# Performance work log

Hardware: AMD Instinct MI355X
Metric: run time of the kernel (lower is better)

Reference implementation:

```python
import jax, jax.numpy as jnp
import numpy as np

B, T, D, L, K = 16, 512, 256, 2, 3
MAX_OUT = 4096  # static padded output length = T * max_duration
LN_EPS = 1e-5


def setup_inputs() -> dict:
    key = jax.random.key(0)
    ks = jax.random.split(key, 8)
    x = jax.random.normal(ks[0], (B, T, D), dtype=jnp.float32)
    mfAlign = jax.random.randint(ks[1], (B, T), 0, 8, dtype=jnp.int32)  # integer frame durations
    pitch = jax.random.uniform(ks[2], (B, T), dtype=jnp.float32)
    energy = jax.random.uniform(ks[3], (B, T), dtype=jnp.float32)
    # duration Predictor params (2 conv layers + layernorms + final linear->1)
    conv_w = jax.random.normal(ks[4], (L, D, D, K), dtype=jnp.float32) * 0.02  # [layer, out, in, k]
    conv_b = jnp.zeros((L, D), dtype=jnp.float32)
    ln_g = jnp.ones((L, D), dtype=jnp.float32)
    ln_b = jnp.zeros((L, D), dtype=jnp.float32)
    lin_w = jax.random.normal(ks[5], (1, D), dtype=jnp.float32) * 0.02
    lin_b = jnp.zeros((1,), dtype=jnp.float32)
    return dict(x=x, mfAlign=mfAlign, pitch=pitch, energy=energy,
                conv_w=conv_w, conv_b=conv_b, ln_g=ln_g, ln_b=ln_b,
                lin_w=lin_w, lin_b=lin_b, max_out=MAX_OUT)


def _conv1d(h, w, b):
    # h: [B, T, D] -> NCW conv with same padding -> [B, T, D]
    y = jax.lax.conv_general_dilated(h.transpose(0, 2, 1), w, (1,), [(K // 2, K // 2)],
                                     dimension_numbers=('NCW', 'OIW', 'NCW'))
    return (y + b[None, :, None]).transpose(0, 2, 1)


def _layernorm(h, g, b):
    m = jnp.mean(h, axis=-1, keepdims=True)
    v = jnp.var(h, axis=-1, keepdims=True)
    return (h - m) * jax.lax.rsqrt(v + LN_EPS) * g + b


def _duration_predictor(h, conv_w, conv_b, ln_g, ln_b, lin_w, lin_b):
    # eval-mode Predictor: conv -> relu -> layernorm (dropout is identity at eval)
    for i in range(conv_w.shape[0]):
        h = _layernorm(jax.nn.relu(_conv1d(h, conv_w[i], conv_b[i])), ln_g[i], ln_b[i])
    return (h @ lin_w.T + lin_b)[..., 0]  # [B, T]


def _length_regulator(x, dur, max_out):
    # expand token t of batch b dur[b,t] times; pad each row to max_out
    dur = jnp.maximum(dur, 0)
    cum = jnp.cumsum(dur, axis=1)                 # [B, T]
    lengths = cum[:, -1]                          # [B]
    pos = jnp.arange(max_out, dtype=cum.dtype)    # [max_out]
    # output frame p of batch b copies token idx[b,p] = first t with cum[b,t] > p
    idx = jax.vmap(lambda c: jnp.searchsorted(c, pos, side='right'))(cum)
    idx = jnp.minimum(idx, x.shape[1] - 1)
    hidden = jnp.take_along_axis(x, idx[:, :, None], axis=1)   # [B, max_out, D]
    mask = (pos[None, :] < lengths[:, None])[:, :, None]
    return jnp.where(mask, hidden, jnp.zeros((), x.dtype)), lengths


def reference(x, mfAlign, pitch, energy, conv_w, conv_b, ln_g, ln_b, lin_w, lin_b, max_out):
    # VarianceAdaptor.forward with bGenerating=False
    lab = mfAlign.astype(x.dtype)
    d = _duration_predictor(jax.lax.stop_gradient(x), conv_w, conv_b, ln_g, ln_b, lin_w, lin_b)
    dLoss = jnp.mean((d - lab) ** 2)
    hiddenSeq, hiddenSeqLength = _length_regulator(x, mfAlign, max_out)
    return hiddenSeq, hiddenSeqLength, dLoss
```

## Files before the change

kernel.cpp:

```cpp
#include <hip/hip_runtime.h>
#include <hip/hip_bf16.h>

#define DD 256
#define TTT 512
#define BB 16
#define KK 3
#define MAXO 4096
#define LN_EPS 1e-5f
#define TPAD 514
#define NKT 24

typedef __attribute__((ext_vector_type(8))) short short8;
typedef __attribute__((ext_vector_type(4))) float f32x4;

static __device__ inline short bf16r(float v) {
    __hip_bfloat16 h = __float2bfloat16(v);
    return reinterpret_cast<short&>(h);
}

__global__ void k_prep_w(const float* __restrict__ w, short* __restrict__ wpk) {
    int tid = blockIdx.x * blockDim.x + threadIdx.x;
    if (tid >= 2 * NKT * 16 * 64) return;
    int lane = tid & 63;
    int rest = tid >> 6;
    int nf = rest & 15; rest >>= 4;
    int kt = rest % NKT;
    int l  = rest / NKT;
    int n     = nf * 16 + (lane & 15);
    int kbase = kt * 32 + (lane >> 4) * 8;
    short8 v;
#pragma unroll
    for (int j = 0; j < 8; ++j) {
        int k   = kbase + j;
        int kap = k >> 8;
        int i   = k & 255;
        v[j] = bf16r(w[(((l * DD) + n) * DD + i) * KK + kap]);
    }
    *reinterpret_cast<short8*>(wpk + (size_t)tid * 8) = v;
}

__global__ void k_prep_x(const float* __restrict__ x, short* __restrict__ xb,
                         short* __restrict__ h1b) {
    int tid = blockIdx.x * blockDim.x + threadIdx.x;
    if (tid >= BB * TPAD * DD) return;
    int r = (tid >> 8) % TPAD;
    if (r == 0 || r == TPAD - 1) {
        xb[tid] = 0; h1b[tid] = 0;
    } else {
        int c = tid & 255;
        int b = tid / (TPAD * DD);
        xb[tid] = bf16r(x[((size_t)b * TTT + (r - 1)) * DD + c]);
    }
}

__global__ void k_cumsum(const int* __restrict__ mf, int* __restrict__ cum,
                         float* __restrict__ dout, int* __restrict__ idxb) {
    __shared__ int s[TTT];
    int b = blockIdx.x, t = threadIdx.x;
    s[t] = mf[b * TTT + t];
    __syncthreads();
    for (int off = 1; off < TTT; off <<= 1) {
        int v = (t >= off) ? s[t - off] : 0;
        __syncthreads();
        s[t] += v;
        __syncthreads();
    }
    cum[b * TTT + t] = s[t];
    int hi = s[t];
    int lo = (t == 0) ? 0 : s[t - 1];
    for (int p = lo; p < hi; ++p) idxb[b * MAXO + p] = t;
    if (t == TTT - 1) dout[(size_t)BB * MAXO * DD + b] = (float)s[t];
    if (b == 0 && t == 0) dout[(size_t)BB * MAXO * DD + BB] = 0.f;
}

template <bool DO_LOSS>
__global__ __launch_bounds__(256) void k_conv_mfma(
    const short* __restrict__ ain,
    short* __restrict__ aout,
    const short8* __restrict__ bp,
    const float* __restrict__ cb,
    const float* __restrict__ g, const float* __restrict__ bvec,
    const float* __restrict__ lw, const float* __restrict__ lb,
    const int* __restrict__ mf, float* __restrict__ loss) {
    __shared__ float yt[16][260];
    int bt = blockIdx.x;
    int b  = bt >> 5;
    int t0 = (bt & 31) << 4;
    int tid = threadIdx.x;
    int lane = tid & 63, wv = tid >> 6;
    int mrow = lane & 15;
    int kg   = lane >> 4;

    const short* Ab = ain + ((size_t)b * TPAD + t0 + mrow) * DD + kg * 8;
    f32x4 acc0 = {0.f,0.f,0.f,0.f}, acc1 = acc0, acc2 = acc0, acc3 = acc0;
    const short8* bw = bp + (size_t)wv * 4 * 64 + lane;

    for (int kt = 0; kt < NKT; ++kt) {
        short8 a  = *reinterpret_cast<const short8*>(Ab + kt * 32);
        short8 b0 = bw[0];
        short8 b1 = bw[64];
        short8 b2 = bw[128];
        short8 b3 = bw[192];
        acc0 = __builtin_amdgcn_mfma_f32_16x16x32_bf16(a, b0, acc0, 0, 0, 0);
        acc1 = __builtin_amdgcn_mfma_f32_16x16x32_bf16(a, b1, acc1, 0, 0, 0);
        acc2 = __builtin_amdgcn_mfma_f32_16x16x32_bf16(a, b2, acc2, 0, 0, 0);
        acc3 = __builtin_amdgcn_mfma_f32_16x16x32_bf16(a, b3, acc3, 0, 0, 0);
        bw += 16 * 64;
    }

#define EPI(F, ACC) { int c = ((wv * 4 + F) << 4) + mrow; float bias = cb[c];   \
        yt[kg * 4 + 0][c] = fmaxf(ACC[0] + bias, 0.f);                          \
        yt[kg * 4 + 1][c] = fmaxf(ACC[1] + bias, 0.f);                          \
        yt[kg * 4 + 2][c] = fmaxf(ACC[2] + bias, 0.f);                          \
        yt[kg * 4 + 3][c] = fmaxf(ACC[3] + bias, 0.f); }
    EPI(0, acc0) EPI(1, acc1) EPI(2, acc2) EPI(3, acc3)
#undef EPI
    __syncthreads();

    float lsum = 0.f;
    int c0 = lane << 1;
#pragma unroll
    for (int q = 0; q < 4; ++q) {
        int r = wv * 4 + q;
        float2 vA = *reinterpret_cast<float2*>(&yt[r][c0]);
        float2 vB = *reinterpret_cast<float2*>(&yt[r][c0 + 128]);
        float s  = vA.x + vA.y + vB.x + vB.y;
        float s2 = vA.x*vA.x + vA.y*vA.y + vB.x*vB.x + vB.y*vB.y;
#pragma unroll
        for (int off = 1; off < 64; off <<= 1) {
            s  += __shfl_xor(s, off);
            s2 += __shfl_xor(s2, off);
        }
        float mean = s * (1.f / DD);
        float var  = s2 * (1.f / DD) - mean * mean;
        float rs   = rsqrtf(var + LN_EPS);
        float2 gA = *reinterpret_cast<const float2*>(&g[c0]);
        float2 gB = *reinterpret_cast<const float2*>(&g[c0 + 128]);
        float2 bA = *reinterpret_cast<const float2*>(&bvec[c0]);
        float2 bB = *reinterpret_cast<const float2*>(&bvec[c0 + 128]);
        float oAx = (vA.x - mean) * rs * gA.x + bA.x;
        float oAy = (vA.y - mean) * rs * gA.y + bA.y;
        float oBx = (vB.x - mean) * rs * gB.x + bB.x;
        float oBy = (vB.y - mean) * rs * gB.y + bB.y;
        if constexpr (!DO_LOSS) {
            size_t rowb = ((size_t)b * TPAD + t0 + r + 1) * DD;
            short2 sA, sB;
            sA.x = bf16r(oAx); sA.y = bf16r(oAy);
            sB.x = bf16r(oBx); sB.y = bf16r(oBy);
            *reinterpret_cast<short2*>(&aout[rowb + c0])       = sA;
            *reinterpret_cast<short2*>(&aout[rowb + c0 + 128]) = sB;
        } else {
            float2 lA = *reinterpret_cast<const float2*>(&lw[c0]);
            float2 lB = *reinterpret_cast<const float2*>(&lw[c0 + 128]);
            float p = oAx * lA.x + oAy * lA.y + oBx * lB.x + oBy * lB.y;
#pragma unroll
            for (int off = 1; off < 64; off <<= 1) p += __shfl_xor(p, off);
            if (lane == 0) {
                float dv = p + lb[0];
                float er = dv - (float)mf[b * TTT + t0 + r];
                lsum += er * er;
            }
        }
    }
    if constexpr (DO_LOSS) {
        if (lane == 0) atomicAdd(loss, lsum * (1.f / (BB * TTT)));
    }
}

__global__ __launch_bounds__(256) void k_lenreg2(const float* __restrict__ x,
                                                 const int* __restrict__ cum,
                                                 const int* __restrict__ idxb,
                                                 float* __restrict__ out) {
    int blk = blockIdx.x;
    int b   = blk >> 7;
    int p0  = (blk & 127) << 5;
    int tid = threadIdx.x;
    int lane = tid & 63, wv = tid >> 6;
    int len = cum[b * TTT + TTT - 1];
    const float4* x4 = (const float4*)x;
    float4* o4 = (float4*)out;
#pragma unroll
    for (int r = 0; r < 8; ++r) {
        int p = p0 + (wv << 3) + r;
        size_t oidx = ((size_t)b * MAXO + p) * 64 + lane;
        if (p < len) {
            int idx = idxb[b * MAXO + p];
            o4[oidx] = x4[((size_t)b * TTT + idx) * 64 + lane];
        } else {
            o4[oidx] = make_float4(0.f, 0.f, 0.f, 0.f);
        }
    }
}

extern "C" void kernel_launch(void* const* d_in, const int* in_sizes, int n_in,
                              void* d_out, int out_size, void* d_ws, size_t ws_size,
                              hipStream_t stream) {
    const float* x      = (const float*)d_in[0];
    const int*   mf     = (const int*)d_in[1];
    const float* conv_w = (const float*)d_in[4];
    const float* conv_b = (const float*)d_in[5];
    const float* ln_g   = (const float*)d_in[6];
    const float* ln_b   = (const float*)d_in[7];
    const float* lin_w  = (const float*)d_in[8];
    const float* lin_b  = (const float*)d_in[9];
    float* out = (float*)d_out;

    short* wpk = (short*)d_ws;
    short* xb  = wpk + (size_t)2 * NKT * 16 * 64 * 8;
    short* h1b = xb + (size_t)BB * TPAD * DD;
    int*   cum  = (int*)(h1b + (size_t)BB * TPAD * DD);
    int*   idxb = cum + BB * TTT;

    float* lossp = out + (size_t)BB * MAXO * DD + BB;

    k_prep_w<<<(2 * NKT * 16 * 64 + 255) / 256, 256, 0, stream>>>(conv_w, wpk);
    k_prep_x<<<(BB * TPAD * DD + 255) / 256, 256, 0, stream>>>(x, xb, h1b);
    k_cumsum<<<BB, TTT, 0, stream>>>(mf, cum, out, idxb);
    k_conv_mfma<false><<<BB * (TTT / 16), 256, 0, stream>>>(
        xb, h1b, (const short8*)wpk, conv_b, ln_g, ln_b,
        nullptr, nullptr, nullptr, nullptr);
    k_conv_mfma<true><<<BB * (TTT / 16), 256, 0, stream>>>(
        h1b, nullptr, (const short8*)wpk + (size_t)NKT * 16 * 64,
        conv_b + DD, ln_g + DD, ln_b + DD, lin_w, lin_b, mf, lossp);
    k_lenreg2<<<BB * (MAXO / 32), 256, 0, stream>>>(x, cum, idxb, out);
}
```

Measured before the change: 165.8 us.

## Merge prep kernels and co-schedule length regulator with first conv layer

```diff
diff --git a/kernel.cpp b/kernel.cpp
--- a/kernel.cpp
+++ b/kernel.cpp
@@ -18,75 +18,71 @@
     return reinterpret_cast<short&>(h);
 }
 
-__global__ void k_prep_w(const float* __restrict__ w, short* __restrict__ wpk) {
-    int tid = blockIdx.x * blockDim.x + threadIdx.x;
-    if (tid >= 2 * NKT * 16 * 64) return;
-    int lane = tid & 63;
-    int rest = tid >> 6;
-    int nf = rest & 15; rest >>= 4;
-    int kt = rest % NKT;
-    int l  = rest / NKT;
-    int n     = nf * 16 + (lane & 15);
-    int kbase = kt * 32 + (lane >> 4) * 8;
-    short8 v;
-#pragma unroll
-    for (int j = 0; j < 8; ++j) {
-        int k   = kbase + j;
-        int kap = k >> 8;
-        int i   = k & 255;
-        v[j] = bf16r(w[(((l * DD) + n) * DD + i) * KK + kap]);
-    }
-    *reinterpret_cast<short8*>(wpk + (size_t)tid * 8) = v;
-}
-
-__global__ void k_prep_x(const float* __restrict__ x, short* __restrict__ xb,
-                         short* __restrict__ h1b) {
-    int tid = blockIdx.x * blockDim.x + threadIdx.x;
-    if (tid >= BB * TPAD * DD) return;
-    int r = (tid >> 8) % TPAD;
-    if (r == 0 || r == TPAD - 1) {
-        xb[tid] = 0; h1b[tid] = 0;
+__global__ __launch_bounds__(512) void k_prep_all(
+    const float* __restrict__ x, const int* __restrict__ mf,
+    const float* __restrict__ w, short* __restrict__ wpk,
+    short* __restrict__ xb, short* __restrict__ h1b,
+    int* __restrict__ cum, int* __restrict__ idxb, float* __restrict__ dout) {
+    __shared__ int s[TTT];
+    int blk = blockIdx.x;
+    if (blk < 16) {
+        int b = blk, t = threadIdx.x;
+        s[t] = mf[b * TTT + t];
+        __syncthreads();
+        for (int off = 1; off < TTT; off <<= 1) {
+            int v = (t >= off) ? s[t - off] : 0;
+            __syncthreads();
+            s[t] += v;
+            __syncthreads();
+        }
+        cum[b * TTT + t] = s[t];
+        int hi = s[t];
+        int lo = (t == 0) ? 0 : s[t - 1];
+        for (int p = lo; p < hi; ++p) idxb[b * MAXO + p] = t;
+        if (t == TTT - 1) dout[(size_t)BB * MAXO * DD + b] = (float)s[t];
+        if (b == 0 && t == 0) dout[(size_t)BB * MAXO * DD + BB] = 0.f;
+    } else if (blk < 112) {
+        int tid = (blk - 16) * 512 + threadIdx.x;
+        int lane = tid & 63;
+        int rest = tid >> 6;
+        int nf = rest & 15; rest >>= 4;
+        int kt = rest % NKT;
+        int l  = rest / NKT;
+        int n     = nf * 16 + (lane & 15);
+        int kbase = kt * 32 + (lane >> 4) * 8;
+        short8 v;
+#pragma unroll
+        for (int j = 0; j < 8; ++j) {
+            int k   = kbase + j;
+            int kap = k >> 8;
+            int i   = k & 255;
+            v[j] = bf16r(w[(((l * DD) + n) * DD + i) * KK + kap]);
+        }
+        *reinterpret_cast<short8*>(wpk + (size_t)tid * 8) = v;
     } else {
-        int c = tid & 255;
-        int b = tid / (TPAD * DD);
-        xb[tid] = bf16r(x[((size_t)b * TTT + (r - 1)) * DD + c]);
-    }
-}
-
-__global__ void k_cumsum(const int* __restrict__ mf, int* __restrict__ cum,
-                         float* __restrict__ dout, int* __restrict__ idxb) {
-    __shared__ int s[TTT];
-    int b = blockIdx.x, t = threadIdx.x;
-    s[t] = mf[b * TTT + t];
-    __syncthreads();
-    for (int off = 1; off < TTT; off <<= 1) {
-        int v = (t >= off) ? s[t - off] : 0;
-        __syncthreads();
-        s[t] += v;
-        __syncthreads();
-    }
-    cum[b * TTT + t] = s[t];
-    int hi = s[t];
-    int lo = (t == 0) ? 0 : s[t - 1];
-    for (int p = lo; p < hi; ++p) idxb[b * MAXO + p] = t;
-    if (t == TTT - 1) dout[(size_t)BB * MAXO * DD + b] = (float)s[t];
-    if (b == 0 && t == 0) dout[(size_t)BB * MAXO * DD + BB] = 0.f;
+        int tid = (blk - 112) * 512 + threadIdx.x;
+        int r = (tid >> 8) % TPAD;
+        if (r == 0 || r == TPAD - 1) {
+            xb[tid] = 0; h1b[tid] = 0;
+        } else {
+            int c = tid & 255;
+            int b = tid / (TPAD * DD);
+            xb[tid] = bf16r(x[((size_t)b * TTT + (r - 1)) * DD + c]);
+        }
+    }
 }
 
 template <bool DO_LOSS>
-__global__ __launch_bounds__(256) void k_conv_mfma(
-    const short* __restrict__ ain,
-    short* __restrict__ aout,
-    const short8* __restrict__ bp,
-    const float* __restrict__ cb,
+static __device__ inline void conv_body(
+    int bt, int tid,
+    const short* __restrict__ ain, short* __restrict__ aout,
+    const short8* __restrict__ bp, const float* __restrict__ cb,
     const float* __restrict__ g, const float* __restrict__ bvec,
     const float* __restrict__ lw, const float* __restrict__ lb,
-    const int* __restrict__ mf, float* __restrict__ loss) {
-    __shared__ float yt[16][260];
-    int bt = blockIdx.x;
+    const int* __restrict__ mf, float* __restrict__ loss,
+    float (*yt)[260]) {
     int b  = bt >> 5;
     int t0 = (bt & 31) << 4;
-    int tid = threadIdx.x;
     int lane = tid & 63, wv = tid >> 6;
     int mrow = lane & 15;
     int kg   = lane >> 4;
@@ -167,29 +163,49 @@
     }
 }
 
-__global__ __launch_bounds__(256) void k_lenreg2(const float* __restrict__ x,
-                                                 const int* __restrict__ cum,
-                                                 const int* __restrict__ idxb,
-                                                 float* __restrict__ out) {
+__global__ __launch_bounds__(256) void k_mid(
+    const short* __restrict__ xb, short* __restrict__ h1b,
+    const short8* __restrict__ bp, const float* __restrict__ cb,
+    const float* __restrict__ g, const float* __restrict__ bvec,
+    const float* __restrict__ x, const int* __restrict__ cum,
+    const int* __restrict__ idxb, float* __restrict__ out) {
+    __shared__ float yt[16][260];
     int blk = blockIdx.x;
-    int b   = blk >> 7;
-    int p0  = (blk & 127) << 5;
     int tid = threadIdx.x;
-    int lane = tid & 63, wv = tid >> 6;
-    int len = cum[b * TTT + TTT - 1];
-    const float4* x4 = (const float4*)x;
-    float4* o4 = (float4*)out;
-#pragma unroll
-    for (int r = 0; r < 8; ++r) {
-        int p = p0 + (wv << 3) + r;
-        size_t oidx = ((size_t)b * MAXO + p) * 64 + lane;
-        if (p < len) {
-            int idx = idxb[b * MAXO + p];
-            o4[oidx] = x4[((size_t)b * TTT + idx) * 64 + lane];
-        } else {
-            o4[oidx] = make_float4(0.f, 0.f, 0.f, 0.f);
-        }
-    }
+    if (blk < 512) {
+        conv_body<false>(blk, tid, xb, h1b, bp, cb, g, bvec,
+                         nullptr, nullptr, nullptr, nullptr, yt);
+    } else {
+        int lrb = blk - 512;
+        int b   = lrb >> 7;
+        int p0  = (lrb & 127) << 5;
+        int lane = tid & 63, wv = tid >> 6;
+        int len = cum[b * TTT + TTT - 1];
+        const float4* x4 = (const float4*)x;
+        float4* o4 = (float4*)out;
+#pragma unroll
+        for (int r = 0; r < 8; ++r) {
+            int p = p0 + (wv << 3) + r;
+            size_t oidx = ((size_t)b * MAXO + p) * 64 + lane;
+            if (p < len) {
+                int idx = idxb[b * MAXO + p];
+                o4[oidx] = x4[((size_t)b * TTT + idx) * 64 + lane];
+            } else {
+                o4[oidx] = make_float4(0.f, 0.f, 0.f, 0.f);
+            }
+        }
+    }
+}
+
+__global__ __launch_bounds__(256) void k_final(
+    const short* __restrict__ h1b, const short8* __restrict__ bp,
+    const float* __restrict__ cb, const float* __restrict__ g,
+    const float* __restrict__ bvec, const float* __restrict__ lw,
+    const float* __restrict__ lb, const int* __restrict__ mf,
+    float* __restrict__ loss) {
+    __shared__ float yt[16][260];
+    conv_body<true>(blockIdx.x, threadIdx.x, h1b, nullptr, bp, cb, g, bvec,
+                    lw, lb, mf, loss, yt);
 }
 
 extern "C" void kernel_launch(void* const* d_in, const int* in_sizes, int n_in,
@@ -213,14 +229,12 @@
 
     float* lossp = out + (size_t)BB * MAXO * DD + BB;
 
-    k_prep_w<<<(2 * NKT * 16 * 64 + 255) / 256, 256, 0, stream>>>(conv_w, wpk);
-    k_prep_x<<<(BB * TPAD * DD + 255) / 256, 256, 0, stream>>>(x, xb, h1b);
-    k_cumsum<<<BB, TTT, 0, stream>>>(mf, cum, out, idxb);
-    k_conv_mfma<false><<<BB * (TTT / 16), 256, 0, stream>>>(
+    k_prep_all<<<16 + 96 + 4112, 512, 0, stream>>>(
+        x, mf, conv_w, wpk, xb, h1b, cum, idxb, out);
+    k_mid<<<512 + BB * (MAXO / 32), 256, 0, stream>>>(
         xb, h1b, (const short8*)wpk, conv_b, ln_g, ln_b,
-        nullptr, nullptr, nullptr, nullptr);
-    k_conv_mfma<true><<<BB * (TTT / 16), 256, 0, stream>>>(
-        h1b, nullptr, (const short8*)wpk + (size_t)NKT * 16 * 64,
+        x, cum, idxb, out);
+    k_final<<<512, 256, 0, stream>>>(
+        h1b, (const short8*)wpk + (size_t)NKT * 16 * 64,
         conv_b + DD, ln_g + DD, ln_b + DD, lin_w, lin_b, mf, lossp);
-    k_lenreg2<<<BB * (MAXO / 32), 256, 0, stream>>>(x, cum, idxb, out);
-}
+}
```

After: 158.6 us. 4.4% less time.
